# Kernel tuning notes

Measured on AMD Instinct MI355X. Metric: run time of the kernel, lower is better.

The kernel has to match this reference:

```python
import jax, jax.numpy as jnp
import numpy as np

B, S, H, D, HID = 2, 2048, 16, 64, 512
INTER = 2 * HID
EPS = 1e-8
SCALE = D ** -0.5
ROPE_THETA = 10000.0


def setup_inputs() -> dict:
    key = jax.random.key(0)
    ks = jax.random.split(key, 12)
    x = jax.random.normal(ks[0], (B, S, HID), dtype=jnp.float32)
    # RoPE tables: angles[s, i] = s / theta^(2i/D), half-dim = D//2
    inv_freq = 1.0 / (ROPE_THETA ** (jnp.arange(0, D, 2, dtype=jnp.float32) / D))  # [D/2]
    ang = jnp.arange(S, dtype=jnp.float32)[:, None] * inv_freq[None, :]            # [S, D/2]
    cos_val = jnp.cos(ang)[None, None]  # [1,1,S,D/2]
    sin_val = jnp.sin(ang)[None, None]
    # additive causal mask
    i = jnp.arange(S)
    causal_mask = jnp.where(i[None, :] > i[:, None], -1e9, 0.0).astype(jnp.float32)[None, None]
    std = 0.02
    wq = jax.random.normal(ks[1], (HID, H * D), dtype=jnp.float32) * std
    wk = jax.random.normal(ks[2], (HID, H * D), dtype=jnp.float32) * std
    wv = jax.random.normal(ks[3], (HID, H * D), dtype=jnp.float32) * std
    wo = jax.random.normal(ks[4], (H * D, HID), dtype=jnp.float32) * std
    w_gate = jax.random.normal(ks[5], (HID, INTER), dtype=jnp.float32) * std
    w_up = jax.random.normal(ks[6], (HID, INTER), dtype=jnp.float32) * std
    w_down = jax.random.normal(ks[7], (INTER, HID), dtype=jnp.float32) * std
    norm1_w = jnp.ones((HID,), dtype=jnp.float32)
    norm2_w = jnp.ones((HID,), dtype=jnp.float32)
    ls_attn = jnp.full((HID,), 0.01, dtype=jnp.float32)
    ls_mlp = jnp.full((HID,), 0.01, dtype=jnp.float32)
    return {"x": x, "cos_val": cos_val, "sin_val": sin_val, "causal_mask": causal_mask,
            "wq": wq, "wk": wk, "wv": wv, "wo": wo,
            "w_gate": w_gate, "w_up": w_up, "w_down": w_down,
            "norm1_w": norm1_w, "norm2_w": norm2_w, "ls_attn": ls_attn, "ls_mlp": ls_mlp}


def _rmsnorm(x, w):
    return x * jax.lax.rsqrt(jnp.mean(x * x, axis=-1, keepdims=True) + EPS) * w


def _rope(t, cos_val, sin_val):
    # t: [B,H,S,D]; rotate-half style with concat halves
    t1, t2 = t[..., : D // 2], t[..., D // 2 :]
    return jnp.concatenate([t1 * cos_val - t2 * sin_val, t2 * cos_val + t1 * sin_val], axis=-1)


def reference(x, cos_val, sin_val, causal_mask, wq, wk, wv, wo,
              w_gate, w_up, w_down, norm1_w, norm2_w, ls_attn, ls_mlp):
    residual = x
    h = _rmsnorm(x, norm1_w)  # [B,S,HID]
    q = (h @ wq).reshape(B, S, H, D).transpose(0, 2, 1, 3)  # [B,H,S,D]
    k = (h @ wk).reshape(B, S, H, D).transpose(0, 2, 1, 3)
    v = (h @ wv).reshape(B, S, H, D).transpose(0, 2, 1, 3)
    q = _rope(q, cos_val, sin_val)
    k = _rope(k, cos_val, sin_val)
    scores = jnp.einsum("bhqd,bhkd->bhqk", q, k) * SCALE + causal_mask
    attn = jax.nn.softmax(scores, axis=-1)
    out = jnp.einsum("bhqk,bhkd->bhqd", attn, v)  # [B,H,S,D]
    out = out.transpose(0, 2, 1, 3).reshape(B, S, H * D)
    attn_out = (out @ wo) * ls_attn  # LayerScale == per-channel scale
    h = residual + attn_out
    residual2 = h
    g = _rmsnorm(h, norm2_w)
    m = jax.nn.silu(g @ w_gate) * (g @ w_up)  # SwiGLU
    m = (m @ w_down) * ls_mlp
    return residual2 + m
```

## Files before the change

kernel.cpp:

```cpp
#include <hip/hip_runtime.h>
#include <hip/hip_bf16.h>

typedef __bf16 bf16x8 __attribute__((ext_vector_type(8)));
typedef __bf16 bf16x4 __attribute__((ext_vector_type(4)));
typedef float f32x4 __attribute__((ext_vector_type(4)));

#define SEQ   2048
#define NB    2
#define NTOK  4096
#define HIDD  512
#define NHEAD 16
#define DHEAD 64
#define QKVN  3072
#define GUN   2048

#define OFF_WQKVT  0u
#define OFF_WOT    3145728u
#define OFF_WGUT   4194304u
#define OFF_WDT    6291456u
#define OFF_HB     7340032u
#define OFF_QKV    11534336u
#define OFF_ATTN   36700160u
#define OFF_H2     45088768u
#define OFF_G      53477376u
#define OFF_M      (OFF_QKV + 16777216u)

#define QSCALE 0.1803368801111731f

#if __has_builtin(__builtin_amdgcn_exp2f)
#define EXP2(x) __builtin_amdgcn_exp2f(x)
#else
#define EXP2(x) exp2f(x)
#endif

typedef unsigned int __attribute__((address_space(1))) as1_uint;
typedef unsigned int __attribute__((address_space(3))) as3_uint;
__device__ __forceinline__ void gload16(const void* g, void* l) {
    __builtin_amdgcn_global_load_lds((const as1_uint*)g, (as3_uint*)l, 16, 0, 0);
}

__global__ __launch_bounds__(256) void prep_k(
    const float* __restrict__ wq, const float* __restrict__ wk,
    const float* __restrict__ wv, const float* __restrict__ wo,
    const float* __restrict__ wg, const float* __restrict__ wu,
    const float* __restrict__ wd,
    __bf16* __restrict__ qkvT, __bf16* __restrict__ woT,
    __bf16* __restrict__ wguT, __bf16* __restrict__ wdT,
    const float* __restrict__ x, const float* __restrict__ norm1,
    __bf16* __restrict__ hb) {
    __shared__ float t[32][33];
    int bid = blockIdx.x;
    if (bid < 3584) {
        int which = bid >> 9, bx = bid & 511;
        const float* in; __bf16* out; int K, N, mode = 0, phase = 0;
        switch (which) {
            case 0: in = wq; out = qkvT;              K = 512;  N = 1024; break;
            case 1: in = wk; out = qkvT + 1024 * 512; K = 512;  N = 1024; break;
            case 2: in = wv; out = qkvT + 2048 * 512; K = 512;  N = 1024; break;
            case 3: in = wo; out = woT;               K = 1024; N = 512;  break;
            case 4: in = wg; out = wguT;              K = 512;  N = 1024; mode = 1; phase = 0; break;
            case 5: in = wu; out = wguT;              K = 512;  N = 1024; mode = 1; phase = 1; break;
            default: in = wd; out = wdT;              K = 1024; N = 512;  break;
        }
        int ntn = N >> 5;
        int n0 = (bx & (ntn - 1)) * 32;
        int k0 = (bx / ntn) * 32;
        int tx = threadIdx.x & 31, ty = threadIdx.x >> 5;
#pragma unroll
        for (int j = 0; j < 4; ++j)
            t[ty * 4 + j][tx] = in[(size_t)(k0 + ty * 4 + j) * N + n0 + tx];
        __syncthreads();
#pragma unroll
        for (int j = 0; j < 4; ++j) {
            int n = n0 + ty * 4 + j;
            int row = mode ? (((n >> 4) << 5) + phase * 16 + (n & 15)) : n;
            out[(size_t)row * K + k0 + tx] = (__bf16)t[tx][ty * 4 + j];
        }
    } else {
        int row = bid - 3584;
        int tt = threadIdx.x;
        const float* xr = x + (size_t)row * HIDD;
        float2 v = *(const float2*)&xr[tt * 2];
        float ss = v.x * v.x + v.y * v.y;
#pragma unroll
        for (int off = 32; off >= 1; off >>= 1) ss += __shfl_xor(ss, off);
        if ((tt & 63) == 0) t[0][tt >> 6] = ss;
        __syncthreads();
        float tot = t[0][0] + t[0][1] + t[0][2] + t[0][3];
        float r = rsqrtf(tot * (1.0f / HIDD) + 1e-8f);
        hb[(size_t)row * HIDD + tt * 2]     = (__bf16)(v.x * r * norm1[tt * 2]);
        hb[(size_t)row * HIDD + tt * 2 + 1] = (__bf16)(v.y * r * norm1[tt * 2 + 1]);
    }
}

__global__ __launch_bounds__(256) void rmsnorm_k(const float* __restrict__ x,
                                                 const float* __restrict__ w,
                                                 __bf16* __restrict__ out) {
    int row = blockIdx.x;
    int t = threadIdx.x;
    const float* xr = x + (size_t)row * HIDD;
    float2 v = *(const float2*)&xr[t * 2];
    float ss = v.x * v.x + v.y * v.y;
#pragma unroll
    for (int off = 32; off >= 1; off >>= 1) ss += __shfl_xor(ss, off);
    __shared__ float red[4];
    if ((t & 63) == 0) red[t >> 6] = ss;
    __syncthreads();
    float tot = red[0] + red[1] + red[2] + red[3];
    float r = rsqrtf(tot * (1.0f / HIDD) + 1e-8f);
    out[(size_t)row * HIDD + t * 2]     = (__bf16)(v.x * r * w[t * 2]);
    out[(size_t)row * HIDD + t * 2 + 1] = (__bf16)(v.y * r * w[t * 2 + 1]);
}

template <int EPI, int TM, int TN, int BK>
__global__ __launch_bounds__(256) void gemm_bt(const __bf16* __restrict__ A,
                                               const __bf16* __restrict__ Bt,
                                               int M, int N, int K,
                                               __bf16* __restrict__ Cb,
                                               float* __restrict__ Cf,
                                               const float* __restrict__ resid,
                                               const float* __restrict__ scale,
                                               const float* __restrict__ cosv,
                                               const float* __restrict__ sinv) {
    __shared__ alignas(16) __bf16 As[TM][BK];
    __shared__ alignas(16) __bf16 Bs[TN][BK];
    constexpr int MI = TM / 32, NI = TN / 32;
    constexpr int CPB = BK / 8;
    int nwg = gridDim.x * gridDim.y;
    int bid = blockIdx.y * gridDim.x + blockIdx.x;
    int swz = (bid & 7) * (nwg >> 3) + (bid >> 3);
    int bx = swz % gridDim.x, by = swz / gridDim.x;
    int m0 = by * TM, n0 = bx * TN;
    int tid = threadIdx.x;
    int lane = tid & 63, w = tid >> 6;
    int wm = (w >> 1) * (TM / 2), wn = (w & 1) * (TN / 2);
    int lr = lane & 15, lkg = lane >> 4;
    f32x4 acc[MI][NI] = {};
    int nkt = K / BK;
    for (int kt = 0; kt < nkt; ++kt) {
        __syncthreads();
#pragma unroll
        for (int i = 0; i < (TM * BK) / 2048; ++i) {
            int c = i * 256 + tid;
            int row = c / CPB, ch = c % CPB;
            gload16(&A[(size_t)(m0 + row) * K + kt * BK + ((ch ^ (row & 7)) << 3)],
                    (__bf16*)As + c * 8);
        }
#pragma unroll
        for (int i = 0; i < (TN * BK) / 2048; ++i) {
            int c = i * 256 + tid;
            int row = c / CPB, ch = c % CPB;
            gload16(&Bt[(size_t)(n0 + row) * K + kt * BK + ((ch ^ (row & 7)) << 3)],
                    (__bf16*)Bs + c * 8);
        }
        __syncthreads();
#pragma unroll
        for (int kk = 0; kk < BK / 32; ++kk) {
            bf16x8 af[MI], bfv[NI];
#pragma unroll
            for (int mi = 0; mi < MI; ++mi) {
                int row = wm + mi * 16 + lr;
                af[mi] = *(const bf16x8*)&As[row][(((kk * 4 + lkg) ^ (row & 7)) << 3)];
            }
#pragma unroll
            for (int ni = 0; ni < NI; ++ni) {
                int row = wn + ni * 16 + lr;
                bfv[ni] = *(const bf16x8*)&Bs[row][(((kk * 4 + lkg) ^ (row & 7)) << 3)];
            }
#pragma unroll
            for (int mi = 0; mi < MI; ++mi)
#pragma unroll
                for (int ni = 0; ni < NI; ++ni)
                    acc[mi][ni] = __builtin_amdgcn_mfma_f32_16x16x32_bf16(
                        af[mi], bfv[ni], acc[mi][ni], 0, 0, 0);
        }
    }
    if (EPI == 1) {
        bool do_rope = (n0 + wn) < 2048;
        float qf = (n0 + wn) < 1024 ? QSCALE : 1.0f;
#pragma unroll
        for (int mi = 0; mi < MI; ++mi)
#pragma unroll
            for (int r = 0; r < 4; ++r) {
                int row = m0 + wm + mi * 16 + (lane >> 4) * 4 + r;
                int s = row & (SEQ - 1);
#pragma unroll
                for (int ni = 0; ni < 2; ++ni) {
                    float v1 = acc[mi][ni][r], v2 = acc[mi][ni + 2][r];
                    size_t i1 = (size_t)row * N + n0 + wn + ni * 16 + lr;
                    size_t i2 = i1 + 32;
                    if (do_rope) {
                        int d = ni * 16 + lr;
                        float c = cosv[s * 32 + d], sn = sinv[s * 32 + d];
                        Cb[i1] = (__bf16)((v1 * c - v2 * sn) * qf);
                        Cb[i2] = (__bf16)((v2 * c + v1 * sn) * qf);
                    } else {
                        Cb[i1] = (__bf16)v1;
                        Cb[i2] = (__bf16)v2;
                    }
                }
            }
    } else if (EPI == 3) {
#pragma unroll
        for (int mi = 0; mi < MI; ++mi)
#pragma unroll
            for (int r = 0; r < 4; ++r) {
                int row = m0 + wm + mi * 16 + (lane >> 4) * 4 + r;
#pragma unroll
                for (int ni = 0; ni < 4; ni += 2) {
                    float g = acc[mi][ni][r], u = acc[mi][ni + 1][r];
                    float mv = (g / (1.0f + __expf(-g))) * u;
                    int j = (((n0 + wn + ni * 16) >> 5) << 4) + lr;
                    Cb[(size_t)row * 1024 + j] = (__bf16)mv;
                }
            }
    } else {
#pragma unroll
        for (int mi = 0; mi < MI; ++mi)
#pragma unroll
            for (int ni = 0; ni < NI; ++ni)
#pragma unroll
                for (int r = 0; r < 4; ++r) {
                    int row = m0 + wm + mi * 16 + (lane >> 4) * 4 + r;
                    int col = n0 + wn + ni * 16 + lr;
                    size_t idx = (size_t)row * N + col;
                    float vv = acc[mi][ni][r];
                    if (EPI == 0) Cb[idx] = (__bf16)vv;
                    else          Cf[idx] = resid[idx] + vv * scale[col];
                }
    }
}

__global__ __launch_bounds__(512, 4) void attn_k(const __bf16* __restrict__ qkv,
                                                 __bf16* __restrict__ outp) {
    __shared__ alignas(16) __bf16 KS[2][2][4096];
    __shared__ alignas(16) __bf16 VS[2][2][4096];
    int bh = blockIdx.x;
    int b = bh >> 4, h = bh & 15;
    int y = blockIdx.y;
    int qbA = y, qbB = 31 - y;
    int TA = y + 1;
    int tid = threadIdx.x;
    int grp = tid >> 8;
    int tg  = tid & 255;
    int lane = tid & 63, wg = tg >> 6;
    int lq = lane & 15, g = lane >> 4;
    size_t tokb = (size_t)b * SEQ;
    int qr0A = qbA * 64 + wg * 16, qr0B = qbB * 64 + wg * 16;

    int vslot = ((lane >> 5) << 2) + ((lane >> 2) & 3);
    int vke   = (((lane >> 4) & 1) << 2) + (lane & 3);

    bf16x8 ones8;
#pragma unroll
    for (int e = 0; e < 8; ++e) ones8[e] = (__bf16)1.0f;

    f32x4 oa[4] = {};
    f32x4 ol = {};
    uint4 vv0, vv1;

#define STAGE_K(kbn, kdst)                                                                         \
    {                                                                                              \
        _Pragma("unroll")                                                                          \
        for (int i = 0; i < 2; ++i) {                                                              \
            int c = i * 256 + tg;                                                                  \
            int kr = c >> 3, sw = c & 7;                                                           \
            gload16(&qkv[(tokb + (kbn) * 64 + kr) * QKVN + 1024 + h * 64 + ((sw ^ (kr & 7)) << 3)], \
                    (kdst) + c * 8);                                                               \
        }                                                                                          \
    }

#define LOAD_V(kbn)                                                                                \
    {                                                                                              \
        const __bf16* vp = &qkv[(tokb + (kbn) * 64 + lane) * QKVN + 2048 + h * 64];                \
        vv0 = *(const uint4*)(vp + (wg * 2) * 8);                                                  \
        vv1 = *(const uint4*)(vp + (wg * 2 + 1) * 8);                                              \
    }

#define WRITE_Vg(vdst)                                                                \
    {                                                                                 \
        const __bf16* ve0 = (const __bf16*)&vv0;                                      \
        const __bf16* ve1 = (const __bf16*)&vv1;                                      \
        _Pragma("unroll")                                                             \
        for (int j = 0; j < 8; ++j) {                                                 \
            int dv0 = (wg * 2) * 8 + j, dv1 = (wg * 2 + 1) * 8 + j;                   \
            (vdst)[dv0 * 64 + ((vslot ^ j) << 3) + vke] = ve0[j];                     \
            (vdst)[dv1 * 64 + ((vslot ^ j) << 3) + vke] = ve1[j];                     \
        }                                                                             \
    }

#define QK_S(sc, aq, ksrc)                                                                         \
    {                                                                                              \
        __builtin_amdgcn_s_setprio(1);                                                             \
        _Pragma("unroll")                                                                          \
        for (int jt = 0; jt < 4; ++jt)                                                             \
            _Pragma("unroll")                                                                      \
            for (int ks = 0; ks < 2; ++ks) {                                                       \
                bf16x8 bk = *(const bf16x8*)&(ksrc)[(jt * 16 + lq) * 64 + (((ks * 4 + g) ^ (lq & 7)) << 3)]; \
                sc[jt] = __builtin_amdgcn_mfma_f32_16x16x32_bf16(bk, aq[ks], sc[jt], 0, 0, 0);     \
            }                                                                                      \
        __builtin_amdgcn_s_setprio(0);                                                             \
    }

#define MASK_S(sc, qr0_t, kb64)                                                                    \
    {                                                                                              \
        int qabs = (qr0_t) + lq;                                                                   \
        _Pragma("unroll")                                                                          \
        for (int jt = 0; jt < 4; ++jt)                                                             \
            _Pragma("unroll")                                                                      \
            for (int r = 0; r < 4; ++r) {                                                          \
                int key = (kb64) * 64 + jt * 16 + g * 4 + r;                                       \
                if (key > qabs) sc[jt][r] = -1e9f;                                                 \
            }                                                                                      \
    }

#define EXP_S(sc)                                                                                  \
    _Pragma("unroll")                                                                              \
    for (int jt = 0; jt < 4; ++jt)                                                                 \
        _Pragma("unroll")                                                                          \
        for (int r = 0; r < 4; ++r) sc[jt][r] = EXP2(sc[jt][r]);

#define PV_S(sc, vsrc)                                                                             \
    {                                                                                              \
        __builtin_amdgcn_s_setprio(1);                                                             \
        _Pragma("unroll")                                                                          \
        for (int ks2 = 0; ks2 < 2; ++ks2) {                                                        \
            bf16x8 pfv;                                                                            \
            _Pragma("unroll")                                                                      \
            for (int e = 0; e < 4; ++e) {                                                          \
                pfv[e]     = (__bf16)sc[2 * ks2][e];                                               \
                pfv[e + 4] = (__bf16)sc[2 * ks2 + 1][e];                                           \
            }                                                                                      \
            ol = __builtin_amdgcn_mfma_f32_16x16x32_bf16(ones8, pfv, ol, 0, 0, 0);                 \
            _Pragma("unroll")                                                                      \
            for (int dt = 0; dt < 4; ++dt) {                                                       \
                bf16x8 av = *(const bf16x8*)&(vsrc)[(dt * 16 + lq) * 64 + (((ks2 * 4 + g) ^ (lq & 7)) << 3)]; \
                oa[dt] = __builtin_amdgcn_mfma_f32_16x16x32_bf16(av, pfv, oa[dt], 0, 0, 0);        \
            }                                                                                      \
        }                                                                                          \
        __builtin_amdgcn_s_setprio(0);                                                             \
    }

    if (grp == 0) {
        bf16x8 aqB[2];
#pragma unroll
        for (int ks = 0; ks < 2; ++ks)
            aqB[ks] = *(const bf16x8*)&qkv[(tokb + qr0B + lq) * QKVN + h * 64 + ks * 32 + g * 8];
        STAGE_K(0, KS[0][0]);
        LOAD_V(0);
        WRITE_Vg(VS[0][0]);
        __syncthreads();
        for (int it = 0; it < 17; ++it) {
            int buf = it & 1;
            bool pf = it < 16;
            if (pf) {
                STAGE_K(it + 1, KS[0][buf ^ 1]);
                LOAD_V(it + 1);
            }
            f32x4 sc[4] = {};
            QK_S(sc, aqB, KS[0][buf]);
            if (it == qbB) MASK_S(sc, qr0B, it);
            EXP_S(sc);
            PV_S(sc, VS[0][buf]);
            if (pf) WRITE_Vg(VS[0][buf ^ 1]);
            __syncthreads();
        }
    } else {
        {
            bf16x8 aqA[2];
#pragma unroll
            for (int ks = 0; ks < 2; ++ks)
                aqA[ks] = *(const bf16x8*)&qkv[(tokb + qr0A + lq) * QKVN + h * 64 + ks * 32 + g * 8];
            __syncthreads();
            for (int it = 0; it < TA; ++it) {
                int buf = it & 1;
                if (it == TA - 1) {
                    STAGE_K(17, KS[1][0]);
                    LOAD_V(17);
                }
                f32x4 sc[4] = {};
                QK_S(sc, aqA, KS[0][buf]);
                if (it == qbA) MASK_S(sc, qr0A, it);
                EXP_S(sc);
                PV_S(sc, VS[0][buf]);
                if (it == TA - 1) WRITE_Vg(VS[1][0]);
                __syncthreads();
            }
        }
        {
            float inv = 1.0f / ol[0];
#pragma unroll
            for (int dt = 0; dt < 4; ++dt) {
                bf16x4 ov;
#pragma unroll
                for (int r = 0; r < 4; ++r) ov[r] = (__bf16)(oa[dt][r] * inv);
                *(bf16x4*)&outp[(tokb + qr0A + lq) * 1024 + h * 64 + dt * 16 + g * 4] = ov;
                oa[dt] = (f32x4){0.f, 0.f, 0.f, 0.f};
            }
            ol = (f32x4){0.f, 0.f, 0.f, 0.f};
        }
        {
            bf16x8 aqB[2];
#pragma unroll
            for (int ks = 0; ks < 2; ++ks)
                aqB[ks] = *(const bf16x8*)&qkv[(tokb + qr0B + lq) * QKVN + h * 64 + ks * 32 + g * 8];
            int cnt = 16 - TA;
            for (int j = 0; j < cnt; ++j) {
                int buf = j & 1;
                if (j + 1 < cnt) {
                    STAGE_K(17 + j + 1, KS[1][buf ^ 1]);
                    LOAD_V(17 + j + 1);
                }
                f32x4 sc[4] = {};
                int kb = 17 + j;
                QK_S(sc, aqB, KS[1][buf]);
                if (kb == qbB) MASK_S(sc, qr0B, kb);
                EXP_S(sc);
                PV_S(sc, VS[1][buf]);
                if (j + 1 < cnt) WRITE_Vg(VS[1][buf ^ 1]);
                __syncthreads();
            }
        }
        __syncthreads();
    }

    float* mrg_oa = (float*)KS[1];
    float* mrg_ol = (float*)VS[1];
    if (grp == 1) {
#pragma unroll
        for (int dt = 0; dt < 4; ++dt)
#pragma unroll
            for (int r = 0; r < 4; ++r) mrg_oa[tg * 16 + dt * 4 + r] = oa[dt][r];
        mrg_ol[tg] = ol[0];
    }
    __syncthreads();
    if (grp == 0) {
        float l = ol[0] + mrg_ol[tg];
        float inv = 1.0f / l;
#pragma unroll
        for (int dt = 0; dt < 4; ++dt) {
            bf16x4 ov;
#pragma unroll
            for (int r = 0; r < 4; ++r)
                ov[r] = (__bf16)((oa[dt][r] + mrg_oa[tg * 16 + dt * 4 + r]) * inv);
            *(bf16x4*)&outp[(tokb + qr0B + lq) * 1024 + h * 64 + dt * 16 + g * 4] = ov;
        }
    }
#undef STAGE_K
#undef LOAD_V
#undef WRITE_Vg
#undef QK_S
#undef MASK_S
#undef EXP_S
#undef PV_S
}

extern "C" void kernel_launch(void* const* d_in, const int* in_sizes, int n_in,
                              void* d_out, int out_size, void* d_ws, size_t ws_size,
                              hipStream_t stream) {
    const float* x       = (const float*)d_in[0];
    const float* cosv    = (const float*)d_in[1];
    const float* sinv    = (const float*)d_in[2];
    const float* wq      = (const float*)d_in[4];
    const float* wk      = (const float*)d_in[5];
    const float* wv      = (const float*)d_in[6];
    const float* wo      = (const float*)d_in[7];
    const float* wgate   = (const float*)d_in[8];
    const float* wup     = (const float*)d_in[9];
    const float* wdown   = (const float*)d_in[10];
    const float* norm1   = (const float*)d_in[11];
    const float* norm2   = (const float*)d_in[12];
    const float* ls_attn = (const float*)d_in[13];
    const float* ls_mlp  = (const float*)d_in[14];

    char* ws = (char*)d_ws;
    __bf16* wqkvT = (__bf16*)(ws + OFF_WQKVT);
    __bf16* woT   = (__bf16*)(ws + OFF_WOT);
    __bf16* wguT  = (__bf16*)(ws + OFF_WGUT);
    __bf16* wdT   = (__bf16*)(ws + OFF_WDT);
    __bf16* hb    = (__bf16*)(ws + OFF_HB);
    __bf16* qkvb  = (__bf16*)(ws + OFF_QKV);
    __bf16* attnb = (__bf16*)(ws + OFF_ATTN);
    float*  h2    = (float*)(ws + OFF_H2);
    __bf16* gb    = (__bf16*)(ws + OFF_G);
    __bf16* mb    = (__bf16*)(ws + OFF_M);
    float*  outf  = (float*)d_out;

    prep_k<<<7680, 256, 0, stream>>>(
        wq, wk, wv, wo, wgate, wup, wdown, wqkvT, woT, wguT, wdT, x, norm1, hb);
    gemm_bt<1, 128, 128, 64><<<dim3(QKVN / 128, NTOK / 128), 256, 0, stream>>>(
        hb, wqkvT, NTOK, QKVN, 512, qkvb, nullptr, nullptr, nullptr, cosv, sinv);
    attn_k<<<dim3(NB * NHEAD, 16), 512, 0, stream>>>(qkvb, attnb);
    gemm_bt<2, 64, 64, 128><<<dim3(HIDD / 64, NTOK / 64), 256, 0, stream>>>(
        attnb, woT, NTOK, HIDD, 1024, nullptr, h2, x, ls_attn, nullptr, nullptr);
    rmsnorm_k<<<NTOK, 256, 0, stream>>>(h2, norm2, gb);
    gemm_bt<3, 128, 128, 64><<<dim3(GUN / 128, NTOK / 128), 256, 0, stream>>>(
        gb, wguT, NTOK, GUN, 512, mb, nullptr, nullptr, nullptr, nullptr, nullptr);
    gemm_bt<2, 64, 64, 128><<<dim3(HIDD / 64, NTOK / 64), 256, 0, stream>>>(
        mb, wdT, NTOK, HIDD, 1024, nullptr, outf, h2, ls_mlp, nullptr, nullptr);
}
```

Before: 112.9 us.

## Pre-transpose K and V into per-head contiguous buffers before attention

Adds a kvprep kernel that copies K into a per-head contiguous layout and writes V transposed and permuted into a per-head buffer. The attention kernel can then stage both K and V with async global-to-LDS 16-byte loads, replacing the register round trip and scattered scalar LDS writes it used for V. The intent is to cut LDS write cost and register pressure inside the attention loop and to let V prefetch overlap compute. The cost is an extra kernel launch plus a full read and write of K and V. The new buffers reuse the workspace regions later used by h2 and m, which are written only after attention has finished.

```diff
diff --git a/kernel.cpp b/kernel.cpp
--- a/kernel.cpp
+++ b/kernel.cpp
@@ -231,7 +231,50 @@
     }
 }
 
+__global__ __launch_bounds__(256) void kvprep_k(const __bf16* __restrict__ qkv,
+                                                __bf16* __restrict__ kb,
+                                                __bf16* __restrict__ vtb) {
+    __shared__ __bf16 tr[64 * 132];
+    int bh = blockIdx.x, st = blockIdx.y;
+    int b = bh >> 4, h = bh & 15;
+    size_t tok0 = (size_t)b * SEQ + st * 128;
+    int tid = threadIdx.x;
+#pragma unroll
+    for (int i = 0; i < 4; ++i) {
+        int c = i * 256 + tid;
+        int kr = c >> 3, ch = c & 7;
+        uint4 v = *(const uint4*)&qkv[(tok0 + kr) * QKVN + 1024 + h * 64 + ch * 8];
+        *(uint4*)&kb[((size_t)bh * SEQ + st * 128 + kr) * 64 + ch * 8] = v;
+    }
+#pragma unroll
+    for (int i = 0; i < 4; ++i) {
+        int c = i * 256 + tid;
+        int vr = c >> 3, ch = c & 7;
+        uint4 v = *(const uint4*)&qkv[(tok0 + vr) * QKVN + 2048 + h * 64 + ch * 8];
+        const __bf16* ve = (const __bf16*)&v;
+#pragma unroll
+        for (int j = 0; j < 8; ++j) tr[(ch * 8 + j) * 132 + vr] = ve[j];
+    }
+    __syncthreads();
+#pragma unroll
+    for (int i = 0; i < 4; ++i) {
+        int c = i * 256 + tid;
+        int dv = c >> 4, rest = c & 15;
+        int t64 = rest >> 3, cc = rest & 7;
+        int K0 = t64 * 64 + 32 * (cc >> 2) + 4 * (cc & 3);
+        __bf16 outv[8];
+#pragma unroll
+        for (int j = 0; j < 4; ++j) outv[j] = tr[dv * 132 + K0 + j];
+#pragma unroll
+        for (int j = 0; j < 4; ++j) outv[4 + j] = tr[dv * 132 + K0 + 16 + j];
+        *(uint4*)&vtb[((size_t)bh * 64 + dv) * SEQ + st * 128 + t64 * 64 + cc * 8] =
+            *(uint4*)outv;
+    }
+}
+
 __global__ __launch_bounds__(512, 4) void attn_k(const __bf16* __restrict__ qkv,
+                                                 const __bf16* __restrict__ kb,
+                                                 const __bf16* __restrict__ vtb,
                                                  __bf16* __restrict__ outp) {
     __shared__ alignas(16) __bf16 KS[2][2][4096];
     __shared__ alignas(16) __bf16 VS[2][2][4096];
@@ -248,45 +291,33 @@
     size_t tokb = (size_t)b * SEQ;
     int qr0A = qbA * 64 + wg * 16, qr0B = qbB * 64 + wg * 16;
 
-    int vslot = ((lane >> 5) << 2) + ((lane >> 2) & 3);
-    int vke   = (((lane >> 4) & 1) << 2) + (lane & 3);
-
     bf16x8 ones8;
 #pragma unroll
     for (int e = 0; e < 8; ++e) ones8[e] = (__bf16)1.0f;
 
     f32x4 oa[4] = {};
     f32x4 ol = {};
-    uint4 vv0, vv1;
 
 #define STAGE_K(kbn, kdst)                                                                         \
     {                                                                                              \
         _Pragma("unroll")                                                                          \
         for (int i = 0; i < 2; ++i) {                                                              \
             int c = i * 256 + tg;                                                                  \
-            int kr = c >> 3, sw = c & 7;                                                           \
-            gload16(&qkv[(tokb + (kbn) * 64 + kr) * QKVN + 1024 + h * 64 + ((sw ^ (kr & 7)) << 3)], \
+            int kr = c >> 3, ch = c & 7;                                                           \
+            gload16(&kb[((size_t)bh * SEQ + (kbn) * 64 + kr) * 64 + ((ch ^ (kr & 7)) << 3)],       \
                     (kdst) + c * 8);                                                               \
         }                                                                                          \
     }
 
-#define LOAD_V(kbn)                                                                                \
+#define STAGE_V(kbn, vdst)                                                                         \
     {                                                                                              \
-        const __bf16* vp = &qkv[(tokb + (kbn) * 64 + lane) * QKVN + 2048 + h * 64];                \
-        vv0 = *(const uint4*)(vp + (wg * 2) * 8);                                                  \
-        vv1 = *(const uint4*)(vp + (wg * 2 + 1) * 8);                                              \
-    }
-
-#define WRITE_Vg(vdst)                                                                \
-    {                                                                                 \
-        const __bf16* ve0 = (const __bf16*)&vv0;                                      \
-        const __bf16* ve1 = (const __bf16*)&vv1;                                      \
-        _Pragma("unroll")                                                             \
-        for (int j = 0; j < 8; ++j) {                                                 \
-            int dv0 = (wg * 2) * 8 + j, dv1 = (wg * 2 + 1) * 8 + j;                   \
-            (vdst)[dv0 * 64 + ((vslot ^ j) << 3) + vke] = ve0[j];                     \
-            (vdst)[dv1 * 64 + ((vslot ^ j) << 3) + vke] = ve1[j];                     \
-        }                                                                             \
+        _Pragma("unroll")                                                                          \
+        for (int i = 0; i < 2; ++i) {                                                              \
+            int c = i * 256 + tg;                                                                  \
+            int vr = c >> 3, ch = c & 7;                                                           \
+            gload16(&vtb[((size_t)bh * 64 + vr) * SEQ + (kbn) * 64 + ((ch ^ (vr & 7)) << 3)],      \
+                    (vdst) + c * 8);                                                               \
+        }                                                                                          \
     }
 
 #define QK_S(sc, aq, ksrc)                                                                         \
@@ -347,22 +378,20 @@
         for (int ks = 0; ks < 2; ++ks)
             aqB[ks] = *(const bf16x8*)&qkv[(tokb + qr0B + lq) * QKVN + h * 64 + ks * 32 + g * 8];
         STAGE_K(0, KS[0][0]);
-        LOAD_V(0);
-        WRITE_Vg(VS[0][0]);
+        STAGE_V(0, VS[0][0]);
         __syncthreads();
         for (int it = 0; it < 17; ++it) {
             int buf = it & 1;
             bool pf = it < 16;
             if (pf) {
                 STAGE_K(it + 1, KS[0][buf ^ 1]);
-                LOAD_V(it + 1);
+                STAGE_V(it + 1, VS[0][buf ^ 1]);
             }
             f32x4 sc[4] = {};
             QK_S(sc, aqB, KS[0][buf]);
             if (it == qbB) MASK_S(sc, qr0B, it);
             EXP_S(sc);
             PV_S(sc, VS[0][buf]);
-            if (pf) WRITE_Vg(VS[0][buf ^ 1]);
             __syncthreads();
         }
     } else {
@@ -376,14 +405,13 @@
                 int buf = it & 1;
                 if (it == TA - 1) {
                     STAGE_K(17, KS[1][0]);
-                    LOAD_V(17);
+                    STAGE_V(17, VS[1][0]);
                 }
                 f32x4 sc[4] = {};
                 QK_S(sc, aqA, KS[0][buf]);
                 if (it == qbA) MASK_S(sc, qr0A, it);
                 EXP_S(sc);
                 PV_S(sc, VS[0][buf]);
-                if (it == TA - 1) WRITE_Vg(VS[1][0]);
                 __syncthreads();
             }
         }
@@ -409,15 +437,14 @@
                 int buf = j & 1;
                 if (j + 1 < cnt) {
                     STAGE_K(17 + j + 1, KS[1][buf ^ 1]);
-                    LOAD_V(17 + j + 1);
+                    STAGE_V(17 + j + 1, VS[1][buf ^ 1]);
                 }
                 f32x4 sc[4] = {};
-                int kb = 17 + j;
+                int kb64 = 17 + j;
                 QK_S(sc, aqB, KS[1][buf]);
-                if (kb == qbB) MASK_S(sc, qr0B, kb);
+                if (kb64 == qbB) MASK_S(sc, qr0B, kb64);
                 EXP_S(sc);
                 PV_S(sc, VS[1][buf]);
-                if (j + 1 < cnt) WRITE_Vg(VS[1][buf ^ 1]);
                 __syncthreads();
             }
         }
@@ -447,8 +474,7 @@
         }
     }
 #undef STAGE_K
-#undef LOAD_V
-#undef WRITE_Vg
+#undef STAGE_V
 #undef QK_S
 #undef MASK_S
 #undef EXP_S
@@ -482,6 +508,8 @@
     __bf16* qkvb  = (__bf16*)(ws + OFF_QKV);
     __bf16* attnb = (__bf16*)(ws + OFF_ATTN);
     float*  h2    = (float*)(ws + OFF_H2);
+    __bf16* kbuf  = (__bf16*)(ws + OFF_H2);
+    __bf16* vtbuf = (__bf16*)(ws + OFF_M);
     __bf16* gb    = (__bf16*)(ws + OFF_G);
     __bf16* mb    = (__bf16*)(ws + OFF_M);
     float*  outf  = (float*)d_out;
@@ -490,7 +518,8 @@
         wq, wk, wv, wo, wgate, wup, wdown, wqkvT, woT, wguT, wdT, x, norm1, hb);
     gemm_bt<1, 128, 128, 64><<<dim3(QKVN / 128, NTOK / 128), 256, 0, stream>>>(
         hb, wqkvT, NTOK, QKVN, 512, qkvb, nullptr, nullptr, nullptr, cosv, sinv);
-    attn_k<<<dim3(NB * NHEAD, 16), 512, 0, stream>>>(qkvb, attnb);
+    kvprep_k<<<dim3(NB * NHEAD, SEQ / 128), 256, 0, stream>>>(qkvb, kbuf, vtbuf);
+    attn_k<<<dim3(NB * NHEAD, 16), 512, 0, stream>>>(qkvb, kbuf, vtbuf, attnb);
     gemm_bt<2, 64, 64, 128><<<dim3(HIDD / 64, NTOK / 64), 256, 0, stream>>>(
         attnb, woT, NTOK, HIDD, 1024, nullptr, h2, x, ls_attn, nullptr, nullptr);
     rmsnorm_k<<<NTOK, 256, 0, stream>>>(h2, norm2, gb);
```

Result: no change. 111.9 us (-1.0%).
